# Performance work log

Hardware: AMD Instinct MI355X
Metric: run time of the kernel (lower is better)

Reference implementation:

```python
import jax, jax.numpy as jnp
import numpy as np

D_MODEL = 1024
NUM_HEADS = 16
HEAD_DIM = D_MODEL // NUM_HEADS
SCALE = HEAD_DIM ** -0.5


def setup_inputs() -> dict:
    key = jax.random.key(0)
    ks = jax.random.split(key, 5)
    B, N = 2, 2048
    x = jax.random.normal(ks[0], (B, N, D_MODEL), dtype=jnp.float32)
    # Linear params, torch layout: weight [out, in], bias [out]
    w_qkv = jax.random.normal(ks[1], (3 * D_MODEL, D_MODEL), dtype=jnp.float32) * (D_MODEL ** -0.5)
    b_qkv = jax.random.normal(ks[2], (3 * D_MODEL,), dtype=jnp.float32) * 0.02
    w_proj = jax.random.normal(ks[3], (D_MODEL, D_MODEL), dtype=jnp.float32) * (D_MODEL ** -0.5)
    b_proj = jax.random.normal(ks[4], (D_MODEL,), dtype=jnp.float32) * 0.02
    return {"x": x, "w_qkv": w_qkv, "b_qkv": b_qkv, "w_proj": w_proj, "b_proj": b_proj}


def reference(x, w_qkv, b_qkv, w_proj, b_proj):
    B, N, C = x.shape
    qkv = x @ w_qkv.T + b_qkv                      # [B, N, 3C]
    qkv = qkv.reshape(B, N, 3, NUM_HEADS, HEAD_DIM)
    qkv = jnp.transpose(qkv, (2, 0, 3, 1, 4))      # [3, B, H, N, d]
    q, k, v = qkv[0], qkv[1], qkv[2]
    attn = jnp.einsum('bhnd,bhmd->bhnm', q, k) * SCALE  # [B, H, N, N]
    attn = jax.nn.softmax(attn, axis=-1)
    # dropout is identity in eval mode
    out = jnp.einsum('bhnm,bhmd->bhnd', attn, v)   # [B, H, N, d]
    out = jnp.transpose(out, (0, 2, 1, 3)).reshape(B, N, C)
    return out @ w_proj.T + b_proj
```

## Files before the change

kernel.cpp:

```cpp
#include <hip/hip_runtime.h>

typedef short short8 __attribute__((ext_vector_type(8)));
typedef short short4v __attribute__((ext_vector_type(4)));
typedef float f32x4 __attribute__((ext_vector_type(4)));
typedef float float4v __attribute__((ext_vector_type(4)));
typedef int int4v __attribute__((ext_vector_type(4)));
typedef int int2v __attribute__((ext_vector_type(2)));

__device__ __forceinline__ short f2bf(float f) {
  union { float f; unsigned u; } v; v.f = f;
  unsigned r = v.u + 0x7FFFu + ((v.u >> 16) & 1u);
  return (short)(r >> 16);
}

__device__ __forceinline__ unsigned cvtpk_bf16(float lo, float hi) {
  unsigned r;
  asm("v_cvt_pk_bf16_f32 %0, %1, %2" : "=v"(r) : "v"(lo), "v"(hi));
  return r;
}

#define GLD16(gp, lp)                                                   \
  __builtin_amdgcn_global_load_lds(                                     \
      (const __attribute__((address_space(1))) void*)(gp),              \
      (__attribute__((address_space(3))) void*)(lp), 16, 0, 0)

#define QSCALE 0.18033688011112042f

__global__ void cvt_f32_bf16(const float* __restrict__ src, short* __restrict__ dst, int n4) {
  int i = blockIdx.x * blockDim.x + threadIdx.x;
  if (i >= n4) return;
  float4v v = ((const float4v*)src)[i];
  short4v o;
  o.x = f2bf(v.x); o.y = f2bf(v.y); o.z = f2bf(v.z); o.w = f2bf(v.w);
  ((short4v*)dst)[i] = o;
}

template <int MODE>
__global__ __launch_bounds__(256) void gemm_bt(
    const short* __restrict__ A, const short* __restrict__ Bw,
    const float* __restrict__ bias,
    short* __restrict__ qo, short* __restrict__ ko, short* __restrict__ vto,
    float* __restrict__ outf) {
  __shared__ short As[2][128 * 64];
  __shared__ short Bs[2][128 * 64];
  const int t = threadIdx.x;
  const int lane = t & 63, wid = t >> 6;
  const int g = lane >> 4, l15 = lane & 15;
  const int wr = (wid >> 1) * 64, wc = (wid & 1) * 64;
  const int bm0 = blockIdx.y * 128, bn0 = blockIdx.x * 128;

  const int sr = t >> 3;
  const int ssub0 = t & 7;

  f32x4 acc[4][4] = {};

  auto stage = [&](int buf, int k0) {
#pragma unroll
    for (int i = 0; i < 4; ++i) {
      int row = i * 32 + sr;
      int s = ssub0 ^ (row & 7);
      char* ldsA = (char*)&As[buf][0] + (i * 256 + (t & ~63)) * 16;
      char* ldsB = (char*)&Bs[buf][0] + (i * 256 + (t & ~63)) * 16;
      GLD16(A + (size_t)(bm0 + row) * 1024 + k0 + s * 8, ldsA);
      GLD16(Bw + (size_t)(bn0 + row) * 1024 + k0 + s * 8, ldsB);
    }
  };

  stage(0, 0);

  for (int it = 0; it < 16; ++it) {
    const int cur = it & 1;
    __syncthreads();
    if (it + 1 < 16) stage(cur ^ 1, (it + 1) * 64);
    const char* AsB = (const char*)&As[cur][0];
    const char* BsB = (const char*)&Bs[cur][0];
#pragma unroll
    for (int kk = 0; kk < 2; ++kk) {
      short8 a[4], b[4];
#pragma unroll
      for (int mi = 0; mi < 4; ++mi) {
        int row = wr + mi * 16 + l15;
        a[mi] = *(const short8*)(AsB + ((row * 128 + kk * 64 + g * 16) ^ ((row & 7) << 4)));
      }
#pragma unroll
      for (int ni = 0; ni < 4; ++ni) {
        int row = wc + ni * 16 + l15;
        b[ni] = *(const short8*)(BsB + ((row * 128 + kk * 64 + g * 16) ^ ((row & 7) << 4)));
      }
#pragma unroll
      for (int mi = 0; mi < 4; ++mi)
#pragma unroll
        for (int ni = 0; ni < 4; ++ni)
          acc[mi][ni] = __builtin_amdgcn_mfma_f32_16x16x32_bf16(a[mi], b[ni], acc[mi][ni], 0, 0, 0);
    }
  }

  if constexpr (MODE == 0) {
    const int which = bn0 >> 10;
    if (which == 2) {
#pragma unroll
      for (int mi = 0; mi < 4; ++mi) {
#pragma unroll
        for (int ni = 0; ni < 4; ++ni) {
          int gcol = bn0 + wc + ni * 16 + l15;
          int w1 = gcol & 1023;
          int h = w1 >> 6, dd = w1 & 63;
          float bv = bias[gcol];
          int grow0 = bm0 + wr + mi * 16 + g * 4;
          int b_ = grow0 >> 11, n0 = grow0 & 2047;
          int bh = b_ * 16 + h;
          int nl = n0 & 63;
          int np = (n0 & ~63) | (nl & 32) | ((nl & 12) << 1) | ((nl & 16) >> 2);
          int2v pk;
          pk.x = (int)cvtpk_bf16(acc[mi][ni][0] + bv, acc[mi][ni][1] + bv);
          pk.y = (int)cvtpk_bf16(acc[mi][ni][2] + bv, acc[mi][ni][3] + bv);
          *(int2v*)(vto + ((size_t)bh * 64 + dd) * 2048 + np) = pk;
        }
      }
    } else {
      short* dst = (which == 0) ? qo : ko;
      const float sc = (which == 0) ? QSCALE : 1.0f;
#pragma unroll
      for (int mi = 0; mi < 4; ++mi) {
#pragma unroll
        for (int ni = 0; ni < 4; ++ni) {
          int gcol = bn0 + wc + ni * 16 + l15;
          int w1 = gcol & 1023;
          int h = w1 >> 6, dd = w1 & 63;
          float bv = bias[gcol];
#pragma unroll
          for (int r = 0; r < 4; ++r) {
            int grow = bm0 + wr + mi * 16 + g * 4 + r;
            int b_ = grow >> 11, n = grow & 2047;
            int bh = b_ * 16 + h;
            dst[((size_t)bh * 2048 + n) * 64 + dd] = f2bf((acc[mi][ni][r] + bv) * sc);
          }
        }
      }
    }
  } else {
#pragma unroll
    for (int mi = 0; mi < 4; ++mi) {
#pragma unroll
      for (int ni = 0; ni < 4; ++ni) {
        int gcol = bn0 + wc + ni * 16 + l15;
        float bv = bias[gcol];
#pragma unroll
        for (int r = 0; r < 4; ++r) {
          int grow = bm0 + wr + mi * 16 + g * 4 + r;
          outf[(size_t)grow * 1024 + gcol] = acc[mi][ni][r] + bv;
        }
      }
    }
  }
}

__global__ __launch_bounds__(256, 2) void attn_fused(
    const short* __restrict__ Qg, const short* __restrict__ Kg,
    const short* __restrict__ Vtg, short* __restrict__ AO) {
  __shared__ short Ks[2][64 * 64];
  __shared__ short Vs[2][64 * 64];
  const int bh = blockIdx.y, qt = blockIdx.x;
  const int t = threadIdx.x, wid = t >> 6, lane = t & 63;
  const int g = lane >> 4, l15 = lane & 15;
  const int q0w = qt * 128 + wid * 32;
  const short* qb = Qg + ((size_t)bh * 2048 + q0w) * 64;
  const short* kb = Kg + (size_t)bh * 2048 * 64;
  const short* vb = Vtg + (size_t)bh * 64 * 2048;

  const int srow = t >> 3;
  const int ssub = (t & 7) ^ (srow & 7);
  const short* ksrc0 = kb + srow * 64 + ssub * 8;
  const short* vsrc0 = vb + (size_t)srow * 2048 + ssub * 8;

  short8 bq[2][2];
#pragma unroll
  for (int qf = 0; qf < 2; ++qf)
#pragma unroll
    for (int kk = 0; kk < 2; ++kk)
      bq[qf][kk] = *(const short8*)(qb + (qf * 16 + l15) * 64 + kk * 32 + g * 8);

#pragma unroll
  for (int i = 0; i < 2; ++i) {
    GLD16(ksrc0 + i * 32 * 64,           (char*)&Ks[0][0] + i * 4096 + wid * 1024);
    GLD16(vsrc0 + (size_t)i * 32 * 2048, (char*)&Vs[0][0] + i * 4096 + wid * 1024);
  }

  f32x4 acc[2][4] = {};
  float mrun[2] = {-3.0e38f, -3.0e38f}, lrun[2] = {0.f, 0.f};

  for (int it = 0; it < 32; ++it) {
    const int cur = it & 1;
    __syncthreads();
    if (it + 1 < 32) {
      const int n1 = (it + 1) * 64;
#pragma unroll
      for (int i = 0; i < 2; ++i) {
        GLD16(ksrc0 + (size_t)(n1 + i * 32) * 64, (char*)&Ks[cur ^ 1][0] + i * 4096 + wid * 1024);
        GLD16(vsrc0 + (size_t)i * 32 * 2048 + n1, (char*)&Vs[cur ^ 1][0] + i * 4096 + wid * 1024);
      }
    }
    const char* KsB = (const char*)&Ks[cur][0];
    const char* VsB = (const char*)&Vs[cur][0];

    f32x4 s[2][4] = {};
#pragma unroll
    for (int kk = 0; kk < 2; ++kk) {
      short8 ak[4];
#pragma unroll
      for (int kf = 0; kf < 4; ++kf) {
        int row = kf * 16 + l15;
        ak[kf] = *(const short8*)(KsB + ((row * 128 + kk * 64 + g * 16) ^ ((row & 7) << 4)));
      }
#pragma unroll
      for (int kf = 0; kf < 4; ++kf)
#pragma unroll
        for (int qf = 0; qf < 2; ++qf)
          s[qf][kf] = __builtin_amdgcn_mfma_f32_16x16x32_bf16(ak[kf], bq[qf][kk], s[qf][kf], 0, 0, 0);
    }

    float pm[2];
#pragma unroll
    for (int qf = 0; qf < 2; ++qf) {
      float m0 = fmaxf(s[qf][0][0], s[qf][0][1]);
      m0 = fmaxf(fmaxf(m0, s[qf][0][2]), s[qf][0][3]);
#pragma unroll
      for (int kf = 1; kf < 4; ++kf) {
        m0 = fmaxf(fmaxf(m0, s[qf][kf][0]), s[qf][kf][1]);
        m0 = fmaxf(fmaxf(m0, s[qf][kf][2]), s[qf][kf][3]);
      }
      float x = fmaxf(m0, __shfl_xor(m0, 16));
      pm[qf] = fmaxf(x, __shfl_xor(x, 32));
    }

    if (!__all((pm[0] - mrun[0] <= 8.f) && (pm[1] - mrun[1] <= 8.f))) {
#pragma unroll
      for (int qf = 0; qf < 2; ++qf) {
        float mn = fmaxf(mrun[qf], pm[qf]);
        float alpha = __builtin_amdgcn_exp2f(mrun[qf] - mn);
        mrun[qf] = mn;
        lrun[qf] *= alpha;
#pragma unroll
        for (int df = 0; df < 4; ++df)
#pragma unroll
          for (int r = 0; r < 4; ++r) acc[qf][df][r] *= alpha;
      }
    }

    unsigned wpk[2][4][2];
#pragma unroll
    for (int qf = 0; qf < 2; ++qf) {
      float rs = 0.f;
      float p[4][4];
#pragma unroll
      for (int kf = 0; kf < 4; ++kf)
#pragma unroll
        for (int r = 0; r < 4; ++r) {
          p[kf][r] = __builtin_amdgcn_exp2f(s[qf][kf][r] - mrun[qf]);
          rs += p[kf][r];
        }
      rs += __shfl_xor(rs, 16);
      rs += __shfl_xor(rs, 32);
      lrun[qf] += rs;
#pragma unroll
      for (int kf = 0; kf < 4; ++kf)
#pragma unroll
        for (int h = 0; h < 2; ++h)
          wpk[qf][kf][h] = cvtpk_bf16(p[kf][2 * h], p[kf][2 * h + 1]);
    }

#pragma unroll
    for (int kk = 0; kk < 2; ++kk) {
      short8 av[4];
#pragma unroll
      for (int df = 0; df < 4; ++df) {
        int row = df * 16 + l15;
        av[df] = *(const short8*)(VsB + ((row * 128 + kk * 64 + g * 16) ^ ((row & 7) << 4)));
      }
#pragma unroll
      for (int qf = 0; qf < 2; ++qf) {
        union { int4v i; short8 s; } pv;
        pv.i[0] = (int)wpk[qf][2 * kk][0];
        pv.i[1] = (int)wpk[qf][2 * kk][1];
        pv.i[2] = (int)wpk[qf][2 * kk + 1][0];
        pv.i[3] = (int)wpk[qf][2 * kk + 1][1];
#pragma unroll
        for (int df = 0; df < 4; ++df)
          acc[qf][df] = __builtin_amdgcn_mfma_f32_16x16x32_bf16(av[df], pv.s, acc[qf][df], 0, 0, 0);
      }
    }
  }

  const int b_ = bh >> 4, h = bh & 15;
#pragma unroll
  for (int qf = 0; qf < 2; ++qf) {
    const float inv = 1.0f / lrun[qf];
    short* outp = AO + ((size_t)b_ * 2048 + q0w + qf * 16 + l15) * 1024 + h * 64 + g * 4;
#pragma unroll
    for (int df = 0; df < 4; ++df) {
      short4v o;
#pragma unroll
      for (int r = 0; r < 4; ++r) o[r] = f2bf(acc[qf][df][r] * inv);
      *(short4v*)(outp + df * 16) = o;
    }
  }
}

extern "C" void kernel_launch(void* const* d_in, const int* in_sizes, int n_in,
                              void* d_out, int out_size, void* d_ws, size_t ws_size,
                              hipStream_t stream) {
  const float* x = (const float*)d_in[0];
  const float* w_qkv = (const float*)d_in[1];
  const float* b_qkv = (const float*)d_in[2];
  const float* w_proj = (const float*)d_in[3];
  const float* b_proj = (const float*)d_in[4];
  float* out = (float*)d_out;
  char* ws = (char*)d_ws;

  short* xb    = (short*)(ws + (size_t)0);
  short* wqkvb = (short*)(ws + ((size_t)8 << 20));
  short* wprojb= (short*)(ws + ((size_t)14 << 20));
  short* qb    = (short*)(ws + ((size_t)16 << 20));
  short* kb    = (short*)(ws + ((size_t)24 << 20));
  short* vtb   = (short*)(ws + ((size_t)32 << 20));
  short* aob   = (short*)(ws + ((size_t)40 << 20));

  cvt_f32_bf16<<<4096, 256, 0, stream>>>(x, xb, 1048576);
  cvt_f32_bf16<<<3072, 256, 0, stream>>>(w_qkv, wqkvb, 786432);
  cvt_f32_bf16<<<1024, 256, 0, stream>>>(w_proj, wprojb, 262144);

  gemm_bt<0><<<dim3(24, 32), 256, 0, stream>>>(xb, wqkvb, b_qkv, qb, kb, vtb, nullptr);
  attn_fused<<<dim3(16, 32), 256, 0, stream>>>(qb, kb, vtb, aob);
  gemm_bt<1><<<dim3(8, 32), 256, 0, stream>>>(aob, wprojb, b_proj, nullptr, nullptr, nullptr, out);
}
```

Measured before the change: 133.6 us.

## Merge conversion kernels, precompute swizzled LDS offsets, remap attention grid order

The three fp32-to-bf16 conversion launches become one kernel that picks its source by index, saving two launches. The GEMM and attention kernels precompute their swizzled LDS fragment offsets once and switch double buffers by XOR-ing a byte offset, which takes address arithmetic out of the inner loops. The attention grid is flattened with batch-head as the fastest index, so concurrently running blocks cover different heads. These are mostly small overhead cuts, and the grid reorder may change L2 locality in either direction.

```diff
diff --git a/kernel.cpp b/kernel.cpp
--- a/kernel.cpp
+++ b/kernel.cpp
@@ -26,13 +26,18 @@
 
 #define QSCALE 0.18033688011112042f
 
-__global__ void cvt_f32_bf16(const float* __restrict__ src, short* __restrict__ dst, int n4) {
-  int i = blockIdx.x * blockDim.x + threadIdx.x;
-  if (i >= n4) return;
-  float4v v = ((const float4v*)src)[i];
+__global__ __launch_bounds__(256) void cvt_all(
+    const float* __restrict__ x, const float* __restrict__ wq, const float* __restrict__ wp,
+    short* __restrict__ xb, short* __restrict__ wqb, short* __restrict__ wpb) {
+  int i = blockIdx.x * 256 + threadIdx.x;
+  const float* s; short* d; int off;
+  if (i < 1048576)      { s = x;  d = xb;  off = i; }
+  else if (i < 1835008) { s = wq; d = wqb; off = i - 1048576; }
+  else                  { s = wp; d = wpb; off = i - 1835008; }
+  float4v v = ((const float4v*)s)[off];
   short4v o;
   o.x = f2bf(v.x); o.y = f2bf(v.y); o.z = f2bf(v.z); o.w = f2bf(v.w);
-  ((short4v*)dst)[i] = o;
+  ((short4v*)d)[off] = o;
 }
 
 template <int MODE>
@@ -52,6 +57,16 @@
   const int sr = t >> 3;
   const int ssub0 = t & 7;
 
+  const int swz = (l15 & 7) << 4;
+  int aoff[2][4], boff[2][4];
+#pragma unroll
+  for (int kk = 0; kk < 2; ++kk)
+#pragma unroll
+    for (int f = 0; f < 4; ++f) {
+      aoff[kk][f] = ((wr + f * 16 + l15) * 128 + kk * 64 + g * 16) ^ swz;
+      boff[kk][f] = ((wc + f * 16 + l15) * 128 + kk * 64 + g * 16) ^ swz;
+    }
+
   f32x4 acc[4][4] = {};
 
   auto stage = [&](int buf, int k0) {
@@ -67,26 +82,21 @@
   };
 
   stage(0, 0);
+  int curOff = 0;
 
   for (int it = 0; it < 16; ++it) {
-    const int cur = it & 1;
     __syncthreads();
-    if (it + 1 < 16) stage(cur ^ 1, (it + 1) * 64);
-    const char* AsB = (const char*)&As[cur][0];
-    const char* BsB = (const char*)&Bs[cur][0];
+    if (it + 1 < 16) stage((it + 1) & 1, (it + 1) * 64);
+    const char* AsB = (const char*)&As[0][0] + curOff;
+    const char* BsB = (const char*)&Bs[0][0] + curOff;
+    curOff ^= 16384;
 #pragma unroll
     for (int kk = 0; kk < 2; ++kk) {
       short8 a[4], b[4];
 #pragma unroll
-      for (int mi = 0; mi < 4; ++mi) {
-        int row = wr + mi * 16 + l15;
-        a[mi] = *(const short8*)(AsB + ((row * 128 + kk * 64 + g * 16) ^ ((row & 7) << 4)));
-      }
-#pragma unroll
-      for (int ni = 0; ni < 4; ++ni) {
-        int row = wc + ni * 16 + l15;
-        b[ni] = *(const short8*)(BsB + ((row * 128 + kk * 64 + g * 16) ^ ((row & 7) << 4)));
-      }
+      for (int mi = 0; mi < 4; ++mi) a[mi] = *(const short8*)(AsB + aoff[kk][mi]);
+#pragma unroll
+      for (int ni = 0; ni < 4; ++ni) b[ni] = *(const short8*)(BsB + boff[kk][ni]);
 #pragma unroll
       for (int mi = 0; mi < 4; ++mi)
 #pragma unroll
@@ -160,7 +170,8 @@
     const short* __restrict__ Vtg, short* __restrict__ AO) {
   __shared__ short Ks[2][64 * 64];
   __shared__ short Vs[2][64 * 64];
-  const int bh = blockIdx.y, qt = blockIdx.x;
+  const int bid = blockIdx.x;
+  const int bh = bid & 31, qt = bid >> 5;
   const int t = threadIdx.x, wid = t >> 6, lane = t & 63;
   const int g = lane >> 4, l15 = lane & 15;
   const int q0w = qt * 128 + wid * 32;
@@ -173,6 +184,14 @@
   const short* ksrc0 = kb + srow * 64 + ssub * 8;
   const short* vsrc0 = vb + (size_t)srow * 2048 + ssub * 8;
 
+  const int swz = (l15 & 7) << 4;
+  int foff[2][4];
+#pragma unroll
+  for (int kk = 0; kk < 2; ++kk)
+#pragma unroll
+    for (int f = 0; f < 4; ++f)
+      foff[kk][f] = ((f * 16 + l15) * 128 + kk * 64 + g * 16) ^ swz;
+
   short8 bq[2][2];
 #pragma unroll
   for (int qf = 0; qf < 2; ++qf)
@@ -188,30 +207,30 @@
 
   f32x4 acc[2][4] = {};
   float mrun[2] = {-3.0e38f, -3.0e38f}, lrun[2] = {0.f, 0.f};
+  int curOff = 0;
 
   for (int it = 0; it < 32; ++it) {
-    const int cur = it & 1;
     __syncthreads();
     if (it + 1 < 32) {
       const int n1 = (it + 1) * 64;
+      char* ldsK = (char*)&Ks[(it + 1) & 1][0] + wid * 1024;
+      char* ldsV = (char*)&Vs[(it + 1) & 1][0] + wid * 1024;
 #pragma unroll
       for (int i = 0; i < 2; ++i) {
-        GLD16(ksrc0 + (size_t)(n1 + i * 32) * 64, (char*)&Ks[cur ^ 1][0] + i * 4096 + wid * 1024);
-        GLD16(vsrc0 + (size_t)i * 32 * 2048 + n1, (char*)&Vs[cur ^ 1][0] + i * 4096 + wid * 1024);
-      }
-    }
-    const char* KsB = (const char*)&Ks[cur][0];
-    const char* VsB = (const char*)&Vs[cur][0];
+        GLD16(ksrc0 + (size_t)(n1 + i * 32) * 64, ldsK + i * 4096);
+        GLD16(vsrc0 + (size_t)i * 32 * 2048 + n1, ldsV + i * 4096);
+      }
+    }
+    const char* KsB = (const char*)&Ks[0][0] + curOff;
+    const char* VsB = (const char*)&Vs[0][0] + curOff;
+    curOff ^= 8192;
 
     f32x4 s[2][4] = {};
 #pragma unroll
     for (int kk = 0; kk < 2; ++kk) {
       short8 ak[4];
 #pragma unroll
-      for (int kf = 0; kf < 4; ++kf) {
-        int row = kf * 16 + l15;
-        ak[kf] = *(const short8*)(KsB + ((row * 128 + kk * 64 + g * 16) ^ ((row & 7) << 4)));
-      }
+      for (int kf = 0; kf < 4; ++kf) ak[kf] = *(const short8*)(KsB + foff[kk][kf]);
 #pragma unroll
       for (int kf = 0; kf < 4; ++kf)
 #pragma unroll
@@ -273,10 +292,7 @@
     for (int kk = 0; kk < 2; ++kk) {
       short8 av[4];
 #pragma unroll
-      for (int df = 0; df < 4; ++df) {
-        int row = df * 16 + l15;
-        av[df] = *(const short8*)(VsB + ((row * 128 + kk * 64 + g * 16) ^ ((row & 7) << 4)));
-      }
+      for (int df = 0; df < 4; ++df) av[df] = *(const short8*)(VsB + foff[kk][df]);
 #pragma unroll
       for (int qf = 0; qf < 2; ++qf) {
         union { int4v i; short8 s; } pv;
@@ -325,11 +341,8 @@
   short* vtb   = (short*)(ws + ((size_t)32 << 20));
   short* aob   = (short*)(ws + ((size_t)40 << 20));
 
-  cvt_f32_bf16<<<4096, 256, 0, stream>>>(x, xb, 1048576);
-  cvt_f32_bf16<<<3072, 256, 0, stream>>>(w_qkv, wqkvb, 786432);
-  cvt_f32_bf16<<<1024, 256, 0, stream>>>(w_proj, wprojb, 262144);
-
+  cvt_all<<<8192, 256, 0, stream>>>(x, w_qkv, w_proj, xb, wqkvb, wprojb);
   gemm_bt<0><<<dim3(24, 32), 256, 0, stream>>>(xb, wqkvb, b_qkv, qb, kb, vtb, nullptr);
-  attn_fused<<<dim3(16, 32), 256, 0, stream>>>(qb, kb, vtb, aob);
+  attn_fused<<<512, 256, 0, stream>>>(qb, kb, vtb, aob);
   gemm_bt<1><<<dim3(8, 32), 256, 0, stream>>>(aob, wprojb, b_proj, nullptr, nullptr, nullptr, out);
 }
```

Measured after the change: 126.8 us. 5.1% less time.
